# Optimization experiments

Measured on AMD Instinct MI355X. Metric: run time of the kernel, lower is better.

Reference implementation:

```python
import jax, jax.numpy as jnp
import numpy as np

N, E, D_IN, D_HID, D_OUT = 100000, 1600000, 128, 128, 40

def _sage_pool(x, src, dst, Wp, bp, Ws, Wn, b, n_nodes):
    # DGL SAGEConv 'pool': h_pool = relu(fc_pool(x)); h_neigh = max over in-neighbors;
    # out = fc_self(x) + fc_neigh(h_neigh) + bias
    hp = jax.nn.relu(x @ Wp + bp)                       # [N, d]
    msg = hp[src]                                        # [E, d] gather
    agg = jax.ops.segment_max(msg, dst, num_segments=n_nodes)  # [N, d] scatter-max
    agg = jnp.where(jnp.isfinite(agg), agg, 0.0)         # zero-in-degree nodes -> 0
    return x @ Ws + agg @ Wn + b

def setup_inputs() -> dict:
    key = jax.random.key(0)
    ks = jax.random.split(key, 14)
    def lin(k, i, o):
        return jax.random.normal(k, (i, o), dtype=jnp.float32) / np.sqrt(i)
    return {
        "in_feat": jax.random.normal(ks[0], (N, D_IN), dtype=jnp.float32),
        "src": jax.random.randint(ks[1], (E,), 0, N),
        "dst": jax.random.randint(ks[2], (E,), 0, N),
        "Wp1": lin(ks[3], D_IN, D_IN), "bp1": jnp.zeros((D_IN,), jnp.float32),
        "Ws1": lin(ks[4], D_IN, D_HID), "Wn1": lin(ks[5], D_IN, D_HID),
        "b1": jnp.zeros((D_HID,), jnp.float32),
        "Wp2": lin(ks[6], D_HID, D_HID), "bp2": jnp.zeros((D_HID,), jnp.float32),
        "Ws2": lin(ks[7], D_HID, D_OUT), "Wn2": lin(ks[8], D_HID, D_OUT),
        "b2": jnp.zeros((D_OUT,), jnp.float32),
    }

def reference(in_feat, src, dst, Wp1, bp1, Ws1, Wn1, b1, Wp2, bp2, Ws2, Wn2, b2):
    h = _sage_pool(in_feat, src, dst, Wp1, bp1, Ws1, Wn1, b1, N)
    h = jax.nn.relu(h)
    # dropout is identity at inference (eval mode)
    return _sage_pool(h, src, dst, Wp2, bp2, Ws2, Wn2, b2, N)
```

## Files before the change

kernel.cpp:

```cpp
#include <hip/hip_runtime.h>
#include <stdint.h>

#define NN 100000
#define NE 1600000
#define NB 391

using u16 = unsigned short;
using u32 = unsigned int;

typedef __attribute__((ext_vector_type(8))) short bf16x8;
typedef __attribute__((ext_vector_type(4))) float f32x4;

__device__ inline u16 f2b(float f){
  u32 u = __float_as_uint(f);
  u32 r = (u + 0x7fffu + ((u >> 16) & 1u)) >> 16;
  return (u16)r;
}

__global__ void k_prep(const float* __restrict__ Wp1, const float* __restrict__ Ws1,
                       const float* __restrict__ Wn1, const float* __restrict__ Wp2,
                       const float* __restrict__ Ws2, const float* __restrict__ Wn2,
                       u16* __restrict__ wpT1, u16* __restrict__ wc1T,
                       u16* __restrict__ wpT2, u16* __restrict__ wc2T){
  int i = blockIdx.x * 256 + threadIdx.x;
  if (i < 16384){ int n = i >> 7, k = i & 127;
    wpT1[n*128 + k] = f2b(Wp1[k*128 + n]);
    wpT2[n*128 + k] = f2b(Wp2[k*128 + n]);
  }
  if (i < 32768){ int n = i >> 8, k = i & 255;
    float v = (k < 128) ? Ws1[k*128 + n] : Wn1[(k-128)*128 + n];
    wc1T[n*256 + k] = f2b(v);
  }
  if (i < 12288){ int n = i >> 8, k = i & 255;
    float v = 0.f;
    if (n < 40) v = (k < 128) ? Ws2[k*40 + n] : Wn2[(k-128)*40 + n];
    wc2T[n*256 + k] = f2b(v);
  }
}

__global__ __launch_bounds__(256) void k_cb_hist(const int* __restrict__ dst,
                                                 int* __restrict__ cb){
  __shared__ int h[NB];
  for (int i = threadIdx.x; i < NB; i += 256) h[i] = 0;
  __syncthreads();
  int e0 = blockIdx.x * 8192;
  #pragma unroll 4
  for (int j = 0; j < 32; j++){
    int e = e0 + j * 256 + threadIdx.x;
    if (e < NE) atomicAdd(&h[dst[e] >> 8], 1);
  }
  __syncthreads();
  for (int i = threadIdx.x; i < NB; i += 256)
    if (h[i]) atomicAdd(&cb[i], h[i]);
}

__global__ void k_cb_scan(const int* __restrict__ cb, int* __restrict__ cbo,
                          int* __restrict__ curB){
  if (threadIdx.x == 0 && blockIdx.x == 0){
    int a = 0;
    for (int i = 0; i < NB; i++){ cbo[i] = a; curB[i] = a; a += cb[i]; }
    cbo[NB] = a;
  }
}

__global__ __launch_bounds__(256) void k_part(const int* __restrict__ src,
                                              const int* __restrict__ dst,
                                              int* __restrict__ curB,
                                              int2* __restrict__ part){
  __shared__ int hist[NB], scn[NB], cur[NB], base[NB];
  __shared__ int2 stage[4096];
  const int tid = threadIdx.x;
  const int e0 = blockIdx.x * 4096;
  const int cnt = min(4096, NE - e0);
  for (int i = tid; i < NB; i += 256) hist[i] = 0;
  __syncthreads();
  int2 ed[16];
  #pragma unroll
  for (int j = 0; j < 16; j++){
    int e = e0 + j * 256 + tid;
    if (e < NE){
      ed[j].x = src[e]; ed[j].y = dst[e];
      atomicAdd(&hist[ed[j].y >> 8], 1);
    }
  }
  __syncthreads();
  for (int i = tid; i < NB; i += 256)
    base[i] = hist[i] ? atomicAdd(&curB[i], hist[i]) : 0;
  if (tid == 0){
    int a = 0;
    for (int i = 0; i < NB; i++){ scn[i] = a; cur[i] = a; a += hist[i]; }
  }
  __syncthreads();
  #pragma unroll
  for (int j = 0; j < 16; j++){
    int e = e0 + j * 256 + tid;
    if (e < NE){
      int slot = atomicAdd(&cur[ed[j].y >> 8], 1);
      stage[slot] = ed[j];
    }
  }
  __syncthreads();
  for (int i = tid; i < cnt; i += 256){
    int2 p = stage[i];
    int b = p.y >> 8;
    part[base[b] + (i - scn[b])] = p;
  }
}

__global__ __launch_bounds__(256) void k_bsort(const int2* __restrict__ part,
                                               const int* __restrict__ cbo,
                                               int* __restrict__ rp,
                                               int* __restrict__ esrc){
  __shared__ int cnt[256], sc[256], cur[256];
  const int tid = threadIdx.x;
  const int b = blockIdx.x;
  const int lo = cbo[b], hi = cbo[b + 1];
  cnt[tid] = 0;
  __syncthreads();
  for (int i = lo + tid; i < hi; i += 256)
    atomicAdd(&cnt[part[i].y & 255], 1);
  __syncthreads();
  sc[tid] = cnt[tid];
  __syncthreads();
  #pragma unroll
  for (int off = 1; off < 256; off <<= 1){
    int t = (tid >= off) ? sc[tid - off] : 0;
    __syncthreads();
    sc[tid] += t;
    __syncthreads();
  }
  int ex = sc[tid] - cnt[tid];
  int n = (b << 8) + tid;
  if (n < NN) rp[n] = lo + ex;
  if (b == NB - 1 && tid == 0) rp[NN] = hi;
  cur[tid] = lo + ex;
  __syncthreads();
  for (int i = lo + tid; i < hi; i += 256){
    int2 p = part[i];
    int pos = atomicAdd(&cur[p.y & 255], 1);
    esrc[pos] = p.x;
  }
}

__global__ void k_agg(const u16* __restrict__ hp, const int* __restrict__ rp,
                      const int* __restrict__ esrc, u16* __restrict__ agg){
  int node = blockIdx.x * 4 + (threadIdx.x >> 6);
  if (node >= NN) return;
  const int lane = threadIdx.x & 63;
  const int half = lane >> 5;
  const int l32  = lane & 31;
  const int lo = rp[node], hi = rp[node + 1];
  u32 m0 = 0, m1 = 0;
  for (int i = lo; i < hi; i += 16){
    int s[8];
    #pragma unroll
    for (int j = 0; j < 8; j++){
      int ii = i + 2 * j + half; if (ii >= hi) ii = hi - 1;
      s[j] = esrc[ii];
    }
    uint2 v[8];
    #pragma unroll
    for (int j = 0; j < 8; j++)
      v[j] = *(const uint2*)&hp[(size_t)s[j] * 128 + l32 * 4];
    #pragma unroll
    for (int j = 0; j < 8; j++){
      asm("v_pk_max_u16 %0, %0, %1" : "+v"(m0) : "v"(v[j].x));
      asm("v_pk_max_u16 %0, %0, %1" : "+v"(m1) : "v"(v[j].y));
    }
  }
  u32 t0 = (u32)__shfl_xor((int)m0, 32);
  u32 t1 = (u32)__shfl_xor((int)m1, 32);
  asm("v_pk_max_u16 %0, %0, %1" : "+v"(m0) : "v"(t0));
  asm("v_pk_max_u16 %0, %0, %1" : "+v"(m1) : "v"(t1));
  if (half == 0)
    *(uint2*)&agg[(size_t)node * 128 + l32 * 4] = make_uint2(m0, m1);
}

template<int K, int NOUT, int NOUTR, int BM, int NT,
         bool A1F32, bool HASA2, bool RELU, bool OUTF32>
__global__ __launch_bounds__(NT)
void k_gemm(const void* __restrict__ A1p, const u16* __restrict__ A2,
            const u16* __restrict__ Wt, const float* __restrict__ bias,
            void* __restrict__ outp)
{
  constexpr int KSTEP = 64;
  constexpr int KP = KSTEP + 8;
  constexpr int NTI = NOUT / 16;
  __shared__ u16 A_lds[BM * KP];
  __shared__ u16 W_lds[NOUT * KP];
  const int tid  = threadIdx.x;
  const int row0 = blockIdx.x * BM;
  const int wave = tid >> 6, lane = tid & 63;
  const int koff = (lane >> 4) * 8;
  const u16* Ar = &A_lds[(wave * 16 + (lane & 15)) * KP];

  f32x4 acc[NTI] = {};

  #pragma unroll
  for (int k0 = 0; k0 < K; k0 += KSTEP){
    if (k0) __syncthreads();
    for (int c = tid; c < NOUT * 8; c += NT){
      int n = c >> 3, kc = c & 7;
      *(uint4*)&W_lds[n * KP + kc * 8] = *(const uint4*)&Wt[n * K + k0 + kc * 8];
    }
    if (A1F32 && k0 < 128){
      const float* A = (const float*)A1p;
      for (int c = tid; c < BM * 16; c += NT){
        int rl = c >> 4, kc = c & 15;
        int gr = row0 + rl;
        float4 v = make_float4(0.f, 0.f, 0.f, 0.f);
        if (gr < NN) v = *(const float4*)&A[(size_t)gr * 128 + k0 + kc * 4];
        ushort4 o; o.x = f2b(v.x); o.y = f2b(v.y); o.z = f2b(v.z); o.w = f2b(v.w);
        *(ushort4*)&A_lds[rl * KP + kc * 4] = o;
      }
    } else {
      const u16* A = (HASA2 && k0 >= 128) ? A2 : (const u16*)A1p;
      int cb = (HASA2 && k0 >= 128) ? (k0 - 128) : k0;
      for (int c = tid; c < BM * 8; c += NT){
        int rl = c >> 3, kc = c & 7;
        int gr = row0 + rl;
        uint4 v = make_uint4(0, 0, 0, 0);
        if (gr < NN) v = *(const uint4*)&A[(size_t)gr * 128 + cb + kc * 8];
        *(uint4*)&A_lds[rl * KP + kc * 8] = v;
      }
    }
    __syncthreads();

    bf16x8 af0 = *(const bf16x8*)&Ar[koff];
    bf16x8 af1 = *(const bf16x8*)&Ar[32 + koff];
    #pragma unroll
    for (int nt = 0; nt < NTI; nt++){
      const u16* Wr = &W_lds[(nt * 16 + (lane & 15)) * KP];
      bf16x8 b0 = *(const bf16x8*)&Wr[koff];
      bf16x8 b1 = *(const bf16x8*)&Wr[32 + koff];
      acc[nt] = __builtin_amdgcn_mfma_f32_16x16x32_bf16(af0, b0, acc[nt], 0, 0, 0);
      acc[nt] = __builtin_amdgcn_mfma_f32_16x16x32_bf16(af1, b1, acc[nt], 0, 0, 0);
    }
  }

  const int colb = lane & 15;
  const int rowl = wave * 16 + ((lane >> 4) << 2);
  #pragma unroll
  for (int nt = 0; nt < NTI; nt++){
    int col = nt * 16 + colb;
    if (col >= NOUTR) continue;
    float bv = bias[col];
    #pragma unroll
    for (int r = 0; r < 4; r++){
      int gr = row0 + rowl + r;
      if (gr >= NN) continue;
      float v = acc[nt][r] + bv;
      if (RELU) v = fmaxf(v, 0.f);
      if (OUTF32) ((float*)outp)[(size_t)gr * NOUTR + col] = v;
      else        ((u16*)outp)[(size_t)gr * NOUTR + col] = f2b(v);
    }
  }
}

extern "C" void kernel_launch(void* const* d_in, const int* in_sizes, int n_in,
                              void* d_out, int out_size, void* d_ws, size_t ws_size,
                              hipStream_t stream){
  const float* x   = (const float*)d_in[0];
  const int*   src = (const int*)d_in[1];
  const int*   dst = (const int*)d_in[2];
  const float* Wp1 = (const float*)d_in[3];
  const float* bp1 = (const float*)d_in[4];
  const float* Ws1 = (const float*)d_in[5];
  const float* Wn1 = (const float*)d_in[6];
  const float* b1  = (const float*)d_in[7];
  const float* Wp2 = (const float*)d_in[8];
  const float* bp2 = (const float*)d_in[9];
  const float* Ws2 = (const float*)d_in[10];
  const float* Wn2 = (const float*)d_in[11];
  const float* b2  = (const float*)d_in[12];

  char* ws = (char*)d_ws;
  u16* wpT1 = (u16*)(ws + 0);
  u16* wc1T = (u16*)(ws + 32768);
  u16* wpT2 = (u16*)(ws + 98304);
  u16* wc2T = (u16*)(ws + 131072);
  int* cb   = (int*)(ws + 155648);
  int* cbo  = (int*)(ws + 157696);
  int* curB = (int*)(ws + 159744);
  int* rp   = (int*)(ws + 161792);
  int2* part= (int2*)(ws + 561920);
  u16* h    = (u16*)(ws + 561920);
  int* esrc = (int*)(ws + 26161920);
  u16* hp   = (u16*)(ws + 32561920);
  u16* agg  = (u16*)(ws + 58161920);

  hipMemsetAsync(cb, 0, NB * sizeof(int), stream);
  k_prep<<<128, 256, 0, stream>>>(Wp1, Ws1, Wn1, Wp2, Ws2, Wn2, wpT1, wc1T, wpT2, wc2T);
  k_cb_hist<<<(NE + 8191) / 8192, 256, 0, stream>>>(dst, cb);
  k_cb_scan<<<1, 64, 0, stream>>>(cb, cbo, curB);
  k_part<<<(NE + 4095) / 4096, 256, 0, stream>>>(src, dst, curB, part);
  k_bsort<<<NB, 256, 0, stream>>>(part, cbo, rp, esrc);

  k_gemm<128,128,128, 64,256, true ,false,true ,false>
      <<<(NN + 63) / 64, 256, 0, stream>>>(x, nullptr, wpT1, bp1, hp);
  k_agg<<<(NN + 3) / 4, 256, 0, stream>>>(hp, rp, esrc, agg);
  k_gemm<256,128,128,128,512, true ,true ,true ,false>
      <<<(NN + 127) / 128, 512, 0, stream>>>(x, agg, wc1T, b1, h);
  k_gemm<128,128,128, 64,256, false,false,true ,false>
      <<<(NN + 63) / 64, 256, 0, stream>>>(h, nullptr, wpT2, bp2, hp);
  k_agg<<<(NN + 3) / 4, 256, 0, stream>>>(hp, rp, esrc, agg);
  k_gemm<256, 48, 40,128,512, false,true ,false,true >
      <<<(NN + 127) / 128, 512, 0, stream>>>(h, agg, wc2T, b2, d_out);
}
```

Measured before the change: 284.1 us.

## Load GEMM A fragments directly from global, widen CSR buckets, parallelize scans

The GEMM kernels stop staging A tiles through LDS. Each lane now loads its MFMA A fragment straight from global memory, converting from fp32 inline where needed, and the full weight matrix is loaded into LDS once per block, which removes the per-K-step barriers. The CSR build moves to 512-node buckets with 512-thread bucket sort, and the serial scans in k_cb_scan and k_part become parallel Hillis-Steele scans. The memset is folded into k_prep. Direct global fragment loads are less coalesced and may raise memory traffic or latency, and the larger LDS weight buffer can reduce occupancy.

```diff
diff --git a/kernel.cpp b/kernel.cpp
--- a/kernel.cpp
+++ b/kernel.cpp
@@ -3,7 +3,7 @@
 
 #define NN 100000
 #define NE 1600000
-#define NB 391
+#define NB 196
 
 using u16 = unsigned short;
 using u32 = unsigned int;
@@ -17,12 +17,25 @@
   return (u16)r;
 }
 
+__device__ inline bf16x8 cvt8(const float* __restrict__ p){
+  float4 a = *(const float4*)p;
+  float4 b = *(const float4*)(p + 4);
+  union { u32 w[4]; bf16x8 v; } u;
+  u.w[0] = (u32)f2b(a.x) | ((u32)f2b(a.y) << 16);
+  u.w[1] = (u32)f2b(a.z) | ((u32)f2b(a.w) << 16);
+  u.w[2] = (u32)f2b(b.x) | ((u32)f2b(b.y) << 16);
+  u.w[3] = (u32)f2b(b.z) | ((u32)f2b(b.w) << 16);
+  return u.v;
+}
+
 __global__ void k_prep(const float* __restrict__ Wp1, const float* __restrict__ Ws1,
                        const float* __restrict__ Wn1, const float* __restrict__ Wp2,
                        const float* __restrict__ Ws2, const float* __restrict__ Wn2,
                        u16* __restrict__ wpT1, u16* __restrict__ wc1T,
-                       u16* __restrict__ wpT2, u16* __restrict__ wc2T){
+                       u16* __restrict__ wpT2, u16* __restrict__ wc2T,
+                       int* __restrict__ cb){
   int i = blockIdx.x * 256 + threadIdx.x;
+  if (i < NB) cb[i] = 0;
   if (i < 16384){ int n = i >> 7, k = i & 127;
     wpT1[n*128 + k] = f2b(Wp1[k*128 + n]);
     wpT2[n*128 + k] = f2b(Wp2[k*128 + n]);
@@ -47,32 +60,43 @@
   #pragma unroll 4
   for (int j = 0; j < 32; j++){
     int e = e0 + j * 256 + threadIdx.x;
-    if (e < NE) atomicAdd(&h[dst[e] >> 8], 1);
+    if (e < NE) atomicAdd(&h[dst[e] >> 9], 1);
   }
   __syncthreads();
   for (int i = threadIdx.x; i < NB; i += 256)
     if (h[i]) atomicAdd(&cb[i], h[i]);
 }
 
-__global__ void k_cb_scan(const int* __restrict__ cb, int* __restrict__ cbo,
-                          int* __restrict__ curB){
-  if (threadIdx.x == 0 && blockIdx.x == 0){
-    int a = 0;
-    for (int i = 0; i < NB; i++){ cbo[i] = a; curB[i] = a; a += cb[i]; }
-    cbo[NB] = a;
-  }
+__global__ __launch_bounds__(256) void k_cb_scan(const int* __restrict__ cb,
+                                                 int* __restrict__ cbo,
+                                                 int* __restrict__ curB){
+  __shared__ int s[256];
+  int tid = threadIdx.x;
+  int v = (tid < NB) ? cb[tid] : 0;
+  s[tid] = v;
+  __syncthreads();
+  #pragma unroll
+  for (int off = 1; off < 256; off <<= 1){
+    int t = (tid >= off) ? s[tid - off] : 0;
+    __syncthreads();
+    s[tid] += t;
+    __syncthreads();
+  }
+  int ex = s[tid] - v;
+  if (tid < NB){ cbo[tid] = ex; curB[tid] = ex; }
+  if (tid == 255) cbo[NB] = s[255];
 }
 
 __global__ __launch_bounds__(256) void k_part(const int* __restrict__ src,
                                               const int* __restrict__ dst,
                                               int* __restrict__ curB,
                                               int2* __restrict__ part){
-  __shared__ int hist[NB], scn[NB], cur[NB], base[NB];
+  __shared__ int hist[256], scn[256], cur[256], base[256];
   __shared__ int2 stage[4096];
   const int tid = threadIdx.x;
   const int e0 = blockIdx.x * 4096;
   const int cnt = min(4096, NE - e0);
-  for (int i = tid; i < NB; i += 256) hist[i] = 0;
+  hist[tid] = 0;
   __syncthreads();
   int2 ed[16];
   #pragma unroll
@@ -80,64 +104,72 @@
     int e = e0 + j * 256 + tid;
     if (e < NE){
       ed[j].x = src[e]; ed[j].y = dst[e];
-      atomicAdd(&hist[ed[j].y >> 8], 1);
-    }
-  }
-  __syncthreads();
-  for (int i = tid; i < NB; i += 256)
-    base[i] = hist[i] ? atomicAdd(&curB[i], hist[i]) : 0;
-  if (tid == 0){
-    int a = 0;
-    for (int i = 0; i < NB; i++){ scn[i] = a; cur[i] = a; a += hist[i]; }
-  }
+      atomicAdd(&hist[ed[j].y >> 9], 1);
+    }
+  }
+  __syncthreads();
+  int hv = hist[tid];
+  base[tid] = (tid < NB && hv) ? atomicAdd(&curB[tid], hv) : 0;
+  scn[tid] = hv;
+  __syncthreads();
+  #pragma unroll
+  for (int off = 1; off < 256; off <<= 1){
+    int t = (tid >= off) ? scn[tid - off] : 0;
+    __syncthreads();
+    scn[tid] += t;
+    __syncthreads();
+  }
+  int ex = scn[tid] - hv;
+  scn[tid] = ex;
+  cur[tid] = ex;
   __syncthreads();
   #pragma unroll
   for (int j = 0; j < 16; j++){
     int e = e0 + j * 256 + tid;
     if (e < NE){
-      int slot = atomicAdd(&cur[ed[j].y >> 8], 1);
+      int slot = atomicAdd(&cur[ed[j].y >> 9], 1);
       stage[slot] = ed[j];
     }
   }
   __syncthreads();
   for (int i = tid; i < cnt; i += 256){
     int2 p = stage[i];
-    int b = p.y >> 8;
+    int b = p.y >> 9;
     part[base[b] + (i - scn[b])] = p;
   }
 }
 
-__global__ __launch_bounds__(256) void k_bsort(const int2* __restrict__ part,
+__global__ __launch_bounds__(512) void k_bsort(const int2* __restrict__ part,
                                                const int* __restrict__ cbo,
                                                int* __restrict__ rp,
                                                int* __restrict__ esrc){
-  __shared__ int cnt[256], sc[256], cur[256];
+  __shared__ int cnt[512], sc[512], cur[512];
   const int tid = threadIdx.x;
   const int b = blockIdx.x;
   const int lo = cbo[b], hi = cbo[b + 1];
   cnt[tid] = 0;
   __syncthreads();
-  for (int i = lo + tid; i < hi; i += 256)
-    atomicAdd(&cnt[part[i].y & 255], 1);
+  for (int i = lo + tid; i < hi; i += 512)
+    atomicAdd(&cnt[part[i].y & 511], 1);
   __syncthreads();
   sc[tid] = cnt[tid];
   __syncthreads();
   #pragma unroll
-  for (int off = 1; off < 256; off <<= 1){
+  for (int off = 1; off < 512; off <<= 1){
     int t = (tid >= off) ? sc[tid - off] : 0;
     __syncthreads();
     sc[tid] += t;
     __syncthreads();
   }
   int ex = sc[tid] - cnt[tid];
-  int n = (b << 8) + tid;
+  int n = (b << 9) + tid;
   if (n < NN) rp[n] = lo + ex;
   if (b == NB - 1 && tid == 0) rp[NN] = hi;
   cur[tid] = lo + ex;
   __syncthreads();
-  for (int i = lo + tid; i < hi; i += 256){
+  for (int i = lo + tid; i < hi; i += 512){
     int2 p = part[i];
-    int pos = atomicAdd(&cur[p.y & 255], 1);
+    int pos = atomicAdd(&cur[p.y & 511], 1);
     esrc[pos] = p.x;
   }
 }
@@ -176,61 +208,48 @@
     *(uint2*)&agg[(size_t)node * 128 + l32 * 4] = make_uint2(m0, m1);
 }
 
-template<int K, int NOUT, int NOUTR, int BM, int NT,
-         bool A1F32, bool HASA2, bool RELU, bool OUTF32>
-__global__ __launch_bounds__(NT)
-void k_gemm(const void* __restrict__ A1p, const u16* __restrict__ A2,
-            const u16* __restrict__ Wt, const float* __restrict__ bias,
-            void* __restrict__ outp)
+template<int K, int NOUT, int NOUTR, bool A1F32, bool HASA2, bool RELU, bool OUTF32>
+__global__ __launch_bounds__(512)
+void k_dgemm(const void* __restrict__ A1p, const u16* __restrict__ A2,
+             const u16* __restrict__ Wt, const float* __restrict__ bias,
+             void* __restrict__ outp)
 {
-  constexpr int KSTEP = 64;
-  constexpr int KP = KSTEP + 8;
+  constexpr int KP  = K + 8;
   constexpr int NTI = NOUT / 16;
-  __shared__ u16 A_lds[BM * KP];
   __shared__ u16 W_lds[NOUT * KP];
   const int tid  = threadIdx.x;
-  const int row0 = blockIdx.x * BM;
+  const int row0 = blockIdx.x * 128;
   const int wave = tid >> 6, lane = tid & 63;
+  const int colb = lane & 15;
   const int koff = (lane >> 4) * 8;
-  const u16* Ar = &A_lds[(wave * 16 + (lane & 15)) * KP];
+
+  for (int c = tid; c < NOUT * (K / 8); c += 512){
+    int n = c / (K / 8), kc = c % (K / 8);
+    *(uint4*)&W_lds[n * KP + kc * 8] = *(const uint4*)&Wt[n * K + kc * 8];
+  }
+  __syncthreads();
+
+  const int rowl = wave * 16 + colb;
+  const int rA   = min(row0 + rowl, NN - 1);
 
   f32x4 acc[NTI] = {};
 
   #pragma unroll
-  for (int k0 = 0; k0 < K; k0 += KSTEP){
-    if (k0) __syncthreads();
-    for (int c = tid; c < NOUT * 8; c += NT){
-      int n = c >> 3, kc = c & 7;
-      *(uint4*)&W_lds[n * KP + kc * 8] = *(const uint4*)&Wt[n * K + k0 + kc * 8];
-    }
+  for (int k0 = 0; k0 < K; k0 += 64){
+    bf16x8 af0, af1;
     if (A1F32 && k0 < 128){
       const float* A = (const float*)A1p;
-      for (int c = tid; c < BM * 16; c += NT){
-        int rl = c >> 4, kc = c & 15;
-        int gr = row0 + rl;
-        float4 v = make_float4(0.f, 0.f, 0.f, 0.f);
-        if (gr < NN) v = *(const float4*)&A[(size_t)gr * 128 + k0 + kc * 4];
-        ushort4 o; o.x = f2b(v.x); o.y = f2b(v.y); o.z = f2b(v.z); o.w = f2b(v.w);
-        *(ushort4*)&A_lds[rl * KP + kc * 4] = o;
-      }
+      af0 = cvt8(&A[(size_t)rA * 128 + k0 + koff]);
+      af1 = cvt8(&A[(size_t)rA * 128 + k0 + 32 + koff]);
     } else {
       const u16* A = (HASA2 && k0 >= 128) ? A2 : (const u16*)A1p;
-      int cb = (HASA2 && k0 >= 128) ? (k0 - 128) : k0;
-      for (int c = tid; c < BM * 8; c += NT){
-        int rl = c >> 3, kc = c & 7;
-        int gr = row0 + rl;
-        uint4 v = make_uint4(0, 0, 0, 0);
-        if (gr < NN) v = *(const uint4*)&A[(size_t)gr * 128 + cb + kc * 8];
-        *(uint4*)&A_lds[rl * KP + kc * 8] = v;
-      }
-    }
-    __syncthreads();
-
-    bf16x8 af0 = *(const bf16x8*)&Ar[koff];
-    bf16x8 af1 = *(const bf16x8*)&Ar[32 + koff];
+      int kb = (HASA2 && k0 >= 128) ? (k0 - 128) : k0;
+      af0 = *(const bf16x8*)&A[(size_t)rA * 128 + kb + koff];
+      af1 = *(const bf16x8*)&A[(size_t)rA * 128 + kb + 32 + koff];
+    }
     #pragma unroll
     for (int nt = 0; nt < NTI; nt++){
-      const u16* Wr = &W_lds[(nt * 16 + (lane & 15)) * KP];
+      const u16* Wr = &W_lds[(nt * 16 + colb) * KP + k0];
       bf16x8 b0 = *(const bf16x8*)&Wr[koff];
       bf16x8 b1 = *(const bf16x8*)&Wr[32 + koff];
       acc[nt] = __builtin_amdgcn_mfma_f32_16x16x32_bf16(af0, b0, acc[nt], 0, 0, 0);
@@ -238,8 +257,7 @@
     }
   }
 
-  const int colb = lane & 15;
-  const int rowl = wave * 16 + ((lane >> 4) << 2);
+  const int rowc = wave * 16 + ((lane >> 4) << 2);
   #pragma unroll
   for (int nt = 0; nt < NTI; nt++){
     int col = nt * 16 + colb;
@@ -247,7 +265,7 @@
     float bv = bias[col];
     #pragma unroll
     for (int r = 0; r < 4; r++){
-      int gr = row0 + rowl + r;
+      int gr = row0 + rowc + r;
       if (gr >= NN) continue;
       float v = acc[nt][r] + bv;
       if (RELU) v = fmaxf(v, 0.f);
@@ -289,21 +307,21 @@
   u16* hp   = (u16*)(ws + 32561920);
   u16* agg  = (u16*)(ws + 58161920);
 
-  hipMemsetAsync(cb, 0, NB * sizeof(int), stream);
-  k_prep<<<128, 256, 0, stream>>>(Wp1, Ws1, Wn1, Wp2, Ws2, Wn2, wpT1, wc1T, wpT2, wc2T);
+  k_prep<<<128, 256, 0, stream>>>(Wp1, Ws1, Wn1, Wp2, Ws2, Wn2,
+                                  wpT1, wc1T, wpT2, wc2T, cb);
   k_cb_hist<<<(NE + 8191) / 8192, 256, 0, stream>>>(dst, cb);
-  k_cb_scan<<<1, 64, 0, stream>>>(cb, cbo, curB);
+  k_cb_scan<<<1, 256, 0, stream>>>(cb, cbo, curB);
   k_part<<<(NE + 4095) / 4096, 256, 0, stream>>>(src, dst, curB, part);
-  k_bsort<<<NB, 256, 0, stream>>>(part, cbo, rp, esrc);
-
-  k_gemm<128,128,128, 64,256, true ,false,true ,false>
-      <<<(NN + 63) / 64, 256, 0, stream>>>(x, nullptr, wpT1, bp1, hp);
+  k_bsort<<<NB, 512, 0, stream>>>(part, cbo, rp, esrc);
+
+  k_dgemm<128,128,128, true ,false,true ,false>
+      <<<(NN + 127) / 128, 512, 0, stream>>>(x, nullptr, wpT1, bp1, hp);
   k_agg<<<(NN + 3) / 4, 256, 0, stream>>>(hp, rp, esrc, agg);
-  k_gemm<256,128,128,128,512, true ,true ,true ,false>
+  k_dgemm<256,128,128, true ,true ,true ,false>
       <<<(NN + 127) / 128, 512, 0, stream>>>(x, agg, wc1T, b1, h);
-  k_gemm<128,128,128, 64,256, false,false,true ,false>
-      <<<(NN + 63) / 64, 256, 0, stream>>>(h, nullptr, wpT2, bp2, hp);
+  k_dgemm<128,128,128, false,false,true ,false>
+      <<<(NN + 127) / 128, 512, 0, stream>>>(h, nullptr, wpT2, bp2, hp);
   k_agg<<<(NN + 3) / 4, 256, 0, stream>>>(hp, rp, esrc, agg);
-  k_gemm<256, 48, 40,128,512, false,true ,false,true >
+  k_dgemm<256, 48, 40, false,true ,false,true >
       <<<(NN + 127) / 128, 512, 0, stream>>>(h, agg, wc2T, b2, d_out);
 }
```

Result: faster. 251.8 us (-11.4%).
